# Performance work log

Measured on AMD Instinct MI355X. Metric: run time of the kernel, lower is better.

Reference implementation:

```python
import jax, jax.numpy as jnp
import numpy as np

B, S, H, D, V = 256, 128, 1024, 256, 1858


def setup_inputs() -> dict:
    key = jax.random.key(0)
    ks = jax.random.split(key, 13)
    s = 1.0 / np.sqrt(H)
    return {
        "hidden_states": jax.random.normal(ks[0], (B, S, H), jnp.float32),
        "Wf": jax.random.normal(ks[1], (D, H), jnp.float32) * s,
        "bf": jax.random.normal(ks[2], (D,), jnp.float32) * 0.01,
        "Wt": jax.random.normal(ks[3], (D, H), jnp.float32) * s,
        "bt": jax.random.normal(ks[4], (D,), jnp.float32) * 0.01,
        "Wg": jax.random.normal(ks[5], (D, H), jnp.float32) * s,
        "bg": jax.random.normal(ks[6], (D,), jnp.float32) * 0.01,
        "promo_tab": jax.random.normal(ks[7], (5, D), jnp.float32),
        "Ws": jax.random.normal(ks[8], (1, D), jnp.float32) * (1.0 / np.sqrt(D)),
        "bs": jax.random.normal(ks[9], (1,), jnp.float32) * 0.01,
        "from_sqs": jax.random.randint(ks[10], (V,), 0, 64, jnp.int32),
        "to_sqs": jax.random.randint(ks[11], (V,), 0, 64, jnp.int32),
        "promo_types": jax.random.randint(ks[12], (V,), 0, 5, jnp.int32),
    }


def reference(hidden_states, Wf, bf, Wt, bt, Wg, bg, promo_tab, Ws, bs,
              from_sqs, to_sqs, promo_types):
    # hidden_states: [B, S, H]; squares are tokens 3:67, global token is 0.
    sq_hidden = hidden_states[:, 3:67, :]          # [B, 64, H]
    global_hidden = hidden_states[:, 0, :]         # [B, H]

    # Linear commutes with gather: project the 64 unique squares first,
    # then gather per move (same math as gather-then-project).
    fp = jnp.einsum('bsh,dh->bsd', sq_hidden, Wf) + bf   # [B, 64, D]
    tp = jnp.einsum('bsh,dh->bsd', sq_hidden, Wt) + bt   # [B, 64, D]
    gp = global_hidden @ Wg.T + bg                       # [B, D]

    from_proj = fp[:, from_sqs, :]                       # [B, V, D]
    to_proj = tp[:, to_sqs, :]                           # [B, V, D]
    promo_feats = promo_tab[promo_types]                 # [V, D]

    combined = from_proj * to_proj + gp[:, None, :] + promo_feats[None]
    # score_proj: Linear(D, 1), then squeeze(-1) -> [B, V]
    return jnp.einsum('bvd,d->bv', jax.nn.relu(combined), Ws[0]) + bs[0]
```

## Files before the change

kernel.cpp:

```cpp
#include <hip/hip_runtime.h>

#define NB   256
#define NSQ  64
#define NH   1024
#define ND   256
#define NV   1858
#define M_   (NB * NSQ)
#define N_   512
#define K_   1024
#define NKT  32

typedef __attribute__((ext_vector_type(4))) float f32x4;
typedef __attribute__((ext_vector_type(8))) short bf16x8;
typedef __attribute__((ext_vector_type(8))) unsigned short u16x8;

__device__ __forceinline__ unsigned short bf16_rne(float x) {
    unsigned u = __float_as_uint(x);
    unsigned r = u + 0x7fffu + ((u >> 16) & 1u);
    return (unsigned short)(r >> 16);
}

__device__ __forceinline__ void gload16(const void* g, void* l) {
    __builtin_amdgcn_global_load_lds(
        (const __attribute__((address_space(1))) unsigned int*)g,
        (__attribute__((address_space(3))) unsigned int*)l, 16, 0, 0);
}

__global__ __launch_bounds__(256) void cast_kernel(
    const float* __restrict__ hid,
    const float* __restrict__ Wf, const float* __restrict__ Wt,
    char* __restrict__ Ahi, char* __restrict__ Alo,
    char* __restrict__ Whi, char* __restrict__ Wlo) {
    int bid = blockIdx.x;
    int tid = threadIdx.x;
    int o = tid * 16;
    int g_l = o >> 10;
    int w = o & 1023;
    int s = w >> 8;
    int r = (w >> 4) & 15;
    const float* src;
    char* dh; char* dl;
    if (bid < 8192) {
        int brow = bid >> 5;
        int kt = bid & 31;
        int m = brow * 64 + g_l * 16 + r;
        int b = m >> 6, sr = m & 63;
        int k = kt * 32 + s * 8;
        src = hid + (size_t)(b * 128 + 3 + sr) * NH + k;
        size_t outb = ((size_t)((brow >> 1) * 32 + kt) << 13) + ((brow & 1) << 12) + o;
        dh = Ahi + outb; dl = Alo + outb;
    } else {
        int bid2 = bid - 8192;
        int nrb = bid2 >> 5;
        int kt = bid2 & 31;
        int n = nrb * 64 + g_l * 16 + r;
        int k = kt * 32 + s * 8;
        src = ((n < ND) ? (Wf + (size_t)n * NH) : (Wt + (size_t)(n - ND) * NH)) + k;
        size_t outb = ((size_t)((nrb >> 1) * 32 + kt) << 13) + ((nrb & 1) << 12) + o;
        dh = Whi + outb; dl = Wlo + outb;
    }
    float4 v0 = ((const float4*)src)[0];
    float4 v1 = ((const float4*)src)[1];
    float vv[8] = {v0.x, v0.y, v0.z, v0.w, v1.x, v1.y, v1.z, v1.w};
    u16x8 h, l;
#pragma unroll
    for (int j = 0; j < 8; ++j) {
        unsigned short hb = bf16_rne(vv[j]);
        float hf = __uint_as_float((unsigned)hb << 16);
        h[j] = hb;
        l[j] = bf16_rne(vv[j] - hf);
    }
    *(u16x8*)dh = h;
    *(u16x8*)dl = l;
}

__global__ __launch_bounds__(1024) void gp_kernel(
    const float* __restrict__ hid, const float* __restrict__ Wg,
    const float* __restrict__ bg, float* __restrict__ gp) {
    __shared__ float h[NH];
    int b = blockIdx.x;
    int tid = threadIdx.x;
    if (tid < 256) ((float4*)h)[tid] = ((const float4*)(hid + (size_t)b * 128 * NH))[tid];
    __syncthreads();
    int wave = tid >> 6, lane = tid & 63;
    const float4* hs = (const float4*)h;
    for (int dd = 0; dd < 16; ++dd) {
        int d = wave * 16 + dd;
        const float4* wrow = (const float4*)(Wg + (size_t)d * NH);
        float acc = 0.f;
#pragma unroll
        for (int p = 0; p < 4; ++p) {
            float4 w = wrow[p * 64 + lane];
            float4 x = hs[p * 64 + lane];
            acc += w.x * x.x + w.y * x.y + w.z * x.z + w.w * x.w;
        }
#pragma unroll
        for (int o = 32; o > 0; o >>= 1) acc += __shfl_xor(acc, o, 64);
        if (lane == 0) gp[(size_t)b * ND + d] = acc + bg[d];
    }
}

__global__ __launch_bounds__(256) void gemm3_kernel(
    const char* __restrict__ Ahi, const char* __restrict__ Alo,
    const char* __restrict__ Whi, const char* __restrict__ Wlo,
    const float* __restrict__ bfv, const float* __restrict__ btv,
    float* __restrict__ C) {
    __shared__ unsigned short lAh[128 * 32], lAl[128 * 32];
    __shared__ unsigned short lBh[128 * 32], lBl[128 * 32];
    int tid = threadIdx.x;
    int wgid = (blockIdx.x & 7) * 64 + (blockIdx.x >> 3);
    int nt = wgid & 3;
    int mt = wgid >> 2;
    int lane = tid & 63, wv = tid >> 6;
    int wm = (wv >> 1) * 64, wn = (wv & 1) * 64;
    int fr = lane & 15, kh = lane >> 4;
    f32x4 acc[4][4] = {};

    for (int kt = 0; kt < NKT; ++kt) {
        size_t ta = (size_t)(mt * NKT + kt) << 13;
        size_t tb = (size_t)(nt * NKT + kt) << 13;
#pragma unroll
        for (int is = 0; is < 2; ++is) {
            int o = is * 4096 + tid * 16;
            gload16(Ahi + ta + o, (char*)lAh + o);
            gload16(Alo + ta + o, (char*)lAl + o);
            gload16(Whi + tb + o, (char*)lBh + o);
            gload16(Wlo + tb + o, (char*)lBl + o);
        }
        __syncthreads();
        bf16x8 ah[4], al[4], bh[4], bl[4];
#pragma unroll
        for (int f = 0; f < 4; ++f) {
            int ea = (wm + f * 16) * 32 + kh * 128 + fr * 8;
            int eb = (wn + f * 16) * 32 + kh * 128 + fr * 8;
            ah[f] = *(const bf16x8*)&lAh[ea];
            al[f] = *(const bf16x8*)&lAl[ea];
            bh[f] = *(const bf16x8*)&lBh[eb];
            bl[f] = *(const bf16x8*)&lBl[eb];
        }
#pragma unroll
        for (int i = 0; i < 4; ++i)
#pragma unroll
            for (int j = 0; j < 4; ++j) {
                acc[i][j] = __builtin_amdgcn_mfma_f32_16x16x32_bf16(ah[i], bh[j], acc[i][j], 0, 0, 0);
                acc[i][j] = __builtin_amdgcn_mfma_f32_16x16x32_bf16(ah[i], bl[j], acc[i][j], 0, 0, 0);
                acc[i][j] = __builtin_amdgcn_mfma_f32_16x16x32_bf16(al[i], bh[j], acc[i][j], 0, 0, 0);
            }
        __syncthreads();
    }

    const float* bias = (nt < 2) ? bfv : btv;
    int nb0 = nt * 128 - ((nt < 2) ? 0 : 256);
#pragma unroll
    for (int j = 0; j < 4; ++j) {
        int ncol = nt * 128 + wn + j * 16 + fr;
        float bv = bias[nb0 + wn + j * 16 + fr];
#pragma unroll
        for (int i = 0; i < 4; ++i) {
            int mrow = mt * 128 + wm + i * 16 + kh * 4;
#pragma unroll
            for (int r = 0; r < 4; ++r) {
                C[(size_t)(mrow + r) * N_ + ncol] = acc[i][j][r] + bv;
            }
        }
    }
}

__global__ __launch_bounds__(1024) void out_kernel(
    const float* __restrict__ C, const float* __restrict__ gp,
    const float* __restrict__ promo_tab, const float* __restrict__ Wsv,
    const float* __restrict__ bsv,
    const int* __restrict__ from_sqs, const int* __restrict__ to_sqs,
    const int* __restrict__ ptypes, float* __restrict__ out) {
    __shared__ float cb[NSQ * N_];
    __shared__ float gpl[ND];
    __shared__ float wsl[ND];
    __shared__ float pl[5 * ND];
    __shared__ int fsq[NV], tsq[NV], pty[NV];
    int b = blockIdx.x;
    int tid = threadIdx.x;
    const float4* src = (const float4*)(C + (size_t)b * NSQ * N_);
    float4* dst = (float4*)cb;
#pragma unroll
    for (int i = 0; i < 8; ++i) dst[tid + i * 1024] = src[tid + i * 1024];
    if (tid < 64) ((float4*)gpl)[tid] = ((const float4*)(gp + (size_t)b * ND))[tid];
    else if (tid < 128) ((float4*)wsl)[tid - 64] = ((const float4*)Wsv)[tid - 64];
    else if (tid < 448) ((float4*)pl)[tid - 128] = ((const float4*)promo_tab)[tid - 128];
    for (int v = tid; v < NV; v += 1024) {
        fsq[v] = from_sqs[v];
        tsq[v] = to_sqs[v];
        pty[v] = ptypes[v];
    }
    __syncthreads();

    int wave = tid >> 6, lane = tid & 63;
    float bias0 = bsv[0];
    const float4* cb4 = (const float4*)cb;
    const float4* gp4 = (const float4*)gpl;
    const float4* ws4 = (const float4*)wsl;
    const float4* pl4 = (const float4*)pl;
    for (int v = wave; v < NV; v += 16) {
        int sf = fsq[v];
        int st = tsq[v];
        int p  = pty[v];
        float4 a = cb4[sf * 128 + lane];
        float4 t = cb4[st * 128 + 64 + lane];
        float4 g = gp4[lane];
        float4 pp = pl4[p * 64 + lane];
        float4 w = ws4[lane];
        float c0 = a.x * t.x + g.x + pp.x;
        float c1 = a.y * t.y + g.y + pp.y;
        float c2 = a.z * t.z + g.z + pp.z;
        float c3 = a.w * t.w + g.w + pp.w;
        float s = fmaxf(c0, 0.f) * w.x + fmaxf(c1, 0.f) * w.y +
                  fmaxf(c2, 0.f) * w.z + fmaxf(c3, 0.f) * w.w;
#pragma unroll
        for (int o = 32; o > 0; o >>= 1) s += __shfl_xor(s, o, 64);
        if (lane == 0) out[(size_t)b * NV + v] = s + bias0;
    }
}

extern "C" void kernel_launch(void* const* d_in, const int* in_sizes, int n_in,
                              void* d_out, int out_size, void* d_ws, size_t ws_size,
                              hipStream_t stream) {
    (void)in_sizes; (void)n_in; (void)out_size; (void)ws_size;
    const float* hid   = (const float*)d_in[0];
    const float* Wf    = (const float*)d_in[1];
    const float* bfv   = (const float*)d_in[2];
    const float* Wt    = (const float*)d_in[3];
    const float* btv   = (const float*)d_in[4];
    const float* Wg    = (const float*)d_in[5];
    const float* bgv   = (const float*)d_in[6];
    const float* promo = (const float*)d_in[7];
    const float* Wsv   = (const float*)d_in[8];
    const float* bsv   = (const float*)d_in[9];
    const int* from_sqs = (const int*)d_in[10];
    const int* to_sqs   = (const int*)d_in[11];
    const int* ptypes   = (const int*)d_in[12];
    float* out = (float*)d_out;

    char* ws = (char*)d_ws;
    char* Ahi = ws;
    char* Alo = ws + 33554432;
    char* Whi = ws + 67108864;
    char* Wlo = ws + 68157440;
    float* C  = (float*)(ws + 69206016);
    float* gp = (float*)(ws + 102760448);

    cast_kernel<<<8448, 256, 0, stream>>>(hid, Wf, Wt, Ahi, Alo, Whi, Wlo);
    gp_kernel<<<256, 1024, 0, stream>>>(hid, Wg, bgv, gp);
    gemm3_kernel<<<512, 256, 0, stream>>>(Ahi, Alo, Whi, Wlo, bfv, btv, C);
    out_kernel<<<256, 1024, 0, stream>>>(C, gp, promo, Wsv, bsv,
                                         from_sqs, to_sqs, ptypes, out);
}
```

Baseline: 336.0 us.

## Pipeline bf16x3 GEMM with triple-buffered LDS and 256x128 tiles

Restructures the split-bf16 GEMM so each 512-thread block computes a 256x128 tile, with 8 waves sharing one B tile. Global-to-LDS loads run through a three-stage ring buffer that prefetches two K-steps ahead. Those loads are interleaved between MFMA groups using barriers, setprio and sched_barrier. The aim is to hide global load latency and cut B-tile traffic, at the cost of 144KB of LDS (one block per CU) and half as many blocks.

```diff
diff --git a/kernel.cpp b/kernel.cpp
--- a/kernel.cpp
+++ b/kernel.cpp
@@ -9,6 +9,7 @@
 #define N_   512
 #define K_   1024
 #define NKT  32
+#define BUFB 49152
 
 typedef __attribute__((ext_vector_type(4))) float f32x4;
 typedef __attribute__((ext_vector_type(8))) short bf16x8;
@@ -100,70 +101,146 @@
     }
 }
 
-__global__ __launch_bounds__(256) void gemm3_kernel(
+__global__ __launch_bounds__(512) void gemm3_kernel(
     const char* __restrict__ Ahi, const char* __restrict__ Alo,
     const char* __restrict__ Whi, const char* __restrict__ Wlo,
     const float* __restrict__ bfv, const float* __restrict__ btv,
     float* __restrict__ C) {
-    __shared__ unsigned short lAh[128 * 32], lAl[128 * 32];
-    __shared__ unsigned short lBh[128 * 32], lBl[128 * 32];
+    __shared__ char lds[3 * BUFB];
     int tid = threadIdx.x;
-    int wgid = (blockIdx.x & 7) * 64 + (blockIdx.x >> 3);
+    int lane = tid & 63, wv = tid >> 6;
+    int wgid = (blockIdx.x & 7) * 32 + (blockIdx.x >> 3);
     int nt = wgid & 3;
     int mt = wgid >> 2;
-    int lane = tid & 63, wv = tid >> 6;
-    int wm = (wv >> 1) * 64, wn = (wv & 1) * 64;
+    int wm = wv >> 1;
+    int wnw = wv & 1;
     int fr = lane & 15, kh = lane >> 4;
+
+    const char* gsrc[6];
+    int loff[6];
+#pragma unroll
+    for (int l = 0; l < 6; ++l) {
+        int seg = wv * 6 + l;
+        const char* base; int lo;
+        if (seg < 8)       { base = Ahi + ((size_t)((2*mt)*NKT) << 13)   + seg*1024;      lo = seg*1024; }
+        else if (seg < 16) { base = Ahi + ((size_t)((2*mt+1)*NKT) << 13) + (seg-8)*1024;  lo = 8192  + (seg-8)*1024; }
+        else if (seg < 24) { base = Alo + ((size_t)((2*mt)*NKT) << 13)   + (seg-16)*1024; lo = 16384 + (seg-16)*1024; }
+        else if (seg < 32) { base = Alo + ((size_t)((2*mt+1)*NKT) << 13) + (seg-24)*1024; lo = 24576 + (seg-24)*1024; }
+        else if (seg < 40) { base = Whi + ((size_t)(nt*NKT) << 13)       + (seg-32)*1024; lo = 32768 + (seg-32)*1024; }
+        else               { base = Wlo + ((size_t)(nt*NKT) << 13)       + (seg-40)*1024; lo = 40960 + (seg-40)*1024; }
+        gsrc[l] = base + lane * 16;
+        loff[l] = lo + lane * 16;
+    }
+
+#define STG(l, ktn, sb) gload16(gsrc[l] + ((size_t)(ktn) << 13), lds + (sb) * BUFB + loff[l])
+
     f32x4 acc[4][4] = {};
 
-    for (int kt = 0; kt < NKT; ++kt) {
-        size_t ta = (size_t)(mt * NKT + kt) << 13;
-        size_t tb = (size_t)(nt * NKT + kt) << 13;
-#pragma unroll
-        for (int is = 0; is < 2; ++is) {
-            int o = is * 4096 + tid * 16;
-            gload16(Ahi + ta + o, (char*)lAh + o);
-            gload16(Alo + ta + o, (char*)lAl + o);
-            gload16(Whi + tb + o, (char*)lBh + o);
-            gload16(Wlo + tb + o, (char*)lBl + o);
-        }
-        __syncthreads();
-        bf16x8 ah[4], al[4], bh[4], bl[4];
-#pragma unroll
-        for (int f = 0; f < 4; ++f) {
-            int ea = (wm + f * 16) * 32 + kh * 128 + fr * 8;
-            int eb = (wn + f * 16) * 32 + kh * 128 + fr * 8;
-            ah[f] = *(const bf16x8*)&lAh[ea];
-            al[f] = *(const bf16x8*)&lAl[ea];
-            bh[f] = *(const bf16x8*)&lBh[eb];
-            bl[f] = *(const bf16x8*)&lBl[eb];
-        }
-#pragma unroll
-        for (int i = 0; i < 4; ++i)
-#pragma unroll
-            for (int j = 0; j < 4; ++j) {
-                acc[i][j] = __builtin_amdgcn_mfma_f32_16x16x32_bf16(ah[i], bh[j], acc[i][j], 0, 0, 0);
-                acc[i][j] = __builtin_amdgcn_mfma_f32_16x16x32_bf16(ah[i], bl[j], acc[i][j], 0, 0, 0);
-                acc[i][j] = __builtin_amdgcn_mfma_f32_16x16x32_bf16(al[i], bh[j], acc[i][j], 0, 0, 0);
-            }
-        __syncthreads();
+#pragma unroll
+    for (int l = 0; l < 6; ++l) STG(l, 0, 0);
+#pragma unroll
+    for (int l = 0; l < 6; ++l) STG(l, 1, 1);
+    asm volatile("s_waitcnt vmcnt(6)" ::: "memory");
+    __builtin_amdgcn_s_barrier();
+    __builtin_amdgcn_sched_barrier(0);
+
+    int rcur = 0, snext = 2;
+    int aoff0 = (wm >> 1) * 8192 + (wm & 1) * 4096 + kh * 256 + fr * 16;
+    int boff0 = 32768 + wnw * 4096 + kh * 256 + fr * 16;
+
+#pragma unroll 1
+    for (int t = 0; t < NKT; ++t) {
+        const char* cb = lds + rcur * BUFB;
+        int ktn = (t + 2) & (NKT - 1);
+        bf16x8 bh[4], bl[4];
+
+#pragma unroll
+        for (int j = 0; j < 4; ++j) {
+            bh[j] = *(const bf16x8*)(cb + boff0 + j * 1024);
+            bl[j] = *(const bf16x8*)(cb + boff0 + 8192 + j * 1024);
+        }
+        bf16x8 ah0 = *(const bf16x8*)(cb + aoff0);
+        bf16x8 al0 = *(const bf16x8*)(cb + 16384 + aoff0);
+        STG(0, ktn, snext); STG(1, ktn, snext);
+        __builtin_amdgcn_s_barrier();
+        __builtin_amdgcn_s_setprio(1);
+#pragma unroll
+        for (int j = 0; j < 4; ++j) {
+            acc[0][j] = __builtin_amdgcn_mfma_f32_16x16x32_bf16(ah0, bh[j], acc[0][j], 0, 0, 0);
+            acc[0][j] = __builtin_amdgcn_mfma_f32_16x16x32_bf16(ah0, bl[j], acc[0][j], 0, 0, 0);
+            acc[0][j] = __builtin_amdgcn_mfma_f32_16x16x32_bf16(al0, bh[j], acc[0][j], 0, 0, 0);
+        }
+        __builtin_amdgcn_s_setprio(0);
+        __builtin_amdgcn_s_barrier();
+        __builtin_amdgcn_sched_barrier(0);
+
+        bf16x8 ah1 = *(const bf16x8*)(cb + aoff0 + 1024);
+        bf16x8 al1 = *(const bf16x8*)(cb + 16384 + aoff0 + 1024);
+        STG(2, ktn, snext); STG(3, ktn, snext);
+        __builtin_amdgcn_s_barrier();
+        __builtin_amdgcn_s_setprio(1);
+#pragma unroll
+        for (int j = 0; j < 4; ++j) {
+            acc[1][j] = __builtin_amdgcn_mfma_f32_16x16x32_bf16(ah1, bh[j], acc[1][j], 0, 0, 0);
+            acc[1][j] = __builtin_amdgcn_mfma_f32_16x16x32_bf16(ah1, bl[j], acc[1][j], 0, 0, 0);
+            acc[1][j] = __builtin_amdgcn_mfma_f32_16x16x32_bf16(al1, bh[j], acc[1][j], 0, 0, 0);
+        }
+        __builtin_amdgcn_s_setprio(0);
+        __builtin_amdgcn_s_barrier();
+        __builtin_amdgcn_sched_barrier(0);
+
+        bf16x8 ah2 = *(const bf16x8*)(cb + aoff0 + 2048);
+        bf16x8 al2 = *(const bf16x8*)(cb + 16384 + aoff0 + 2048);
+        STG(4, ktn, snext);
+        __builtin_amdgcn_s_barrier();
+        __builtin_amdgcn_s_setprio(1);
+#pragma unroll
+        for (int j = 0; j < 4; ++j) {
+            acc[2][j] = __builtin_amdgcn_mfma_f32_16x16x32_bf16(ah2, bh[j], acc[2][j], 0, 0, 0);
+            acc[2][j] = __builtin_amdgcn_mfma_f32_16x16x32_bf16(ah2, bl[j], acc[2][j], 0, 0, 0);
+            acc[2][j] = __builtin_amdgcn_mfma_f32_16x16x32_bf16(al2, bh[j], acc[2][j], 0, 0, 0);
+        }
+        __builtin_amdgcn_s_setprio(0);
+        __builtin_amdgcn_s_barrier();
+        __builtin_amdgcn_sched_barrier(0);
+
+        bf16x8 ah3 = *(const bf16x8*)(cb + aoff0 + 3072);
+        bf16x8 al3 = *(const bf16x8*)(cb + 16384 + aoff0 + 3072);
+        STG(5, ktn, snext);
+        __builtin_amdgcn_s_barrier();
+        __builtin_amdgcn_s_setprio(1);
+#pragma unroll
+        for (int j = 0; j < 4; ++j) {
+            acc[3][j] = __builtin_amdgcn_mfma_f32_16x16x32_bf16(ah3, bh[j], acc[3][j], 0, 0, 0);
+            acc[3][j] = __builtin_amdgcn_mfma_f32_16x16x32_bf16(ah3, bl[j], acc[3][j], 0, 0, 0);
+            acc[3][j] = __builtin_amdgcn_mfma_f32_16x16x32_bf16(al3, bh[j], acc[3][j], 0, 0, 0);
+        }
+        __builtin_amdgcn_s_setprio(0);
+        asm volatile("s_waitcnt vmcnt(6)" ::: "memory");
+        __builtin_amdgcn_s_barrier();
+        __builtin_amdgcn_sched_barrier(0);
+
+        rcur = (rcur == 2) ? 0 : rcur + 1;
+        snext = (snext == 2) ? 0 : snext + 1;
     }
 
     const float* bias = (nt < 2) ? bfv : btv;
     int nb0 = nt * 128 - ((nt < 2) ? 0 : 256);
 #pragma unroll
     for (int j = 0; j < 4; ++j) {
-        int ncol = nt * 128 + wn + j * 16 + fr;
-        float bv = bias[nb0 + wn + j * 16 + fr];
+        int nc = wnw * 64 + j * 16 + fr;
+        int ncol = nt * 128 + nc;
+        float bv = bias[nb0 + nc];
 #pragma unroll
         for (int i = 0; i < 4; ++i) {
-            int mrow = mt * 128 + wm + i * 16 + kh * 4;
+            int mrow = mt * 256 + wm * 64 + i * 16 + kh * 4;
 #pragma unroll
             for (int r = 0; r < 4; ++r) {
                 C[(size_t)(mrow + r) * N_ + ncol] = acc[i][j][r] + bv;
             }
         }
     }
+#undef STG
 }
 
 __global__ __launch_bounds__(1024) void out_kernel(
@@ -249,7 +326,7 @@
 
     cast_kernel<<<8448, 256, 0, stream>>>(hid, Wf, Wt, Ahi, Alo, Whi, Wlo);
     gp_kernel<<<256, 1024, 0, stream>>>(hid, Wg, bgv, gp);
-    gemm3_kernel<<<512, 256, 0, stream>>>(Ahi, Alo, Whi, Wlo, bfv, btv, C);
+    gemm3_kernel<<<256, 512, 0, stream>>>(Ahi, Alo, Whi, Wlo, bfv, btv, C);
     out_kernel<<<256, 1024, 0, stream>>>(C, gp, promo, Wsv, bsv,
                                          from_sqs, to_sqs, ptypes, out);
 }
```

Measured after the change: 334.4 us. No clear change (-0.5%).

## Fuse activation cast, GEMM and scoring into one per-batch kernel

Applied to the files above, without the earlier changes.

Removes the separate activation cast pass and the C intermediate buffer. One block per batch now converts hidden rows to bf16 hi/lo pairs in registers, writes them to LDS, and runs a double-buffered split-bf16 MFMA GEMM for all 512 output columns. It then keeps the projections in LDS for the gather/ReLU/dot scoring stage. This cuts global traffic heavily, but only 256 blocks of 512 threads with about 144KB of LDS each can run, so occupancy drops and each block does much more serial work.

```diff
diff --git a/kernel.cpp b/kernel.cpp
--- a/kernel.cpp
+++ b/kernel.cpp
@@ -5,9 +5,7 @@
 #define NH   1024
 #define ND   256
 #define NV   1858
-#define M_   (NB * NSQ)
 #define N_   512
-#define K_   1024
 #define NKT  32
 
 typedef __attribute__((ext_vector_type(4))) float f32x4;
@@ -26,10 +24,8 @@
         (__attribute__((address_space(3))) unsigned int*)l, 16, 0, 0);
 }
 
-__global__ __launch_bounds__(256) void cast_kernel(
-    const float* __restrict__ hid,
+__global__ __launch_bounds__(256) void cast_W_kernel(
     const float* __restrict__ Wf, const float* __restrict__ Wt,
-    char* __restrict__ Ahi, char* __restrict__ Alo,
     char* __restrict__ Whi, char* __restrict__ Wlo) {
     int bid = blockIdx.x;
     int tid = threadIdx.x;
@@ -38,27 +34,11 @@
     int w = o & 1023;
     int s = w >> 8;
     int r = (w >> 4) & 15;
-    const float* src;
-    char* dh; char* dl;
-    if (bid < 8192) {
-        int brow = bid >> 5;
-        int kt = bid & 31;
-        int m = brow * 64 + g_l * 16 + r;
-        int b = m >> 6, sr = m & 63;
-        int k = kt * 32 + s * 8;
-        src = hid + (size_t)(b * 128 + 3 + sr) * NH + k;
-        size_t outb = ((size_t)((brow >> 1) * 32 + kt) << 13) + ((brow & 1) << 12) + o;
-        dh = Ahi + outb; dl = Alo + outb;
-    } else {
-        int bid2 = bid - 8192;
-        int nrb = bid2 >> 5;
-        int kt = bid2 & 31;
-        int n = nrb * 64 + g_l * 16 + r;
-        int k = kt * 32 + s * 8;
-        src = ((n < ND) ? (Wf + (size_t)n * NH) : (Wt + (size_t)(n - ND) * NH)) + k;
-        size_t outb = ((size_t)((nrb >> 1) * 32 + kt) << 13) + ((nrb & 1) << 12) + o;
-        dh = Whi + outb; dl = Wlo + outb;
-    }
+    int nrb = bid >> 5, kt = bid & 31;
+    int n = nrb * 64 + g_l * 16 + r;
+    int k = kt * 32 + s * 8;
+    const float* src = ((n < ND) ? (Wf + (size_t)n * NH) : (Wt + (size_t)(n - ND) * NH)) + k;
+    size_t outb = ((size_t)((nrb >> 1) * 32 + kt) << 13) + ((nrb & 1) << 12) + o;
     float4 v0 = ((const float4*)src)[0];
     float4 v1 = ((const float4*)src)[1];
     float vv[8] = {v0.x, v0.y, v0.z, v0.w, v1.x, v1.y, v1.z, v1.w};
@@ -70,8 +50,8 @@
         h[j] = hb;
         l[j] = bf16_rne(vv[j] - hf);
     }
-    *(u16x8*)dh = h;
-    *(u16x8*)dl = l;
+    *(u16x8*)(Whi + outb) = h;
+    *(u16x8*)(Wlo + outb) = l;
 }
 
 __global__ __launch_bounds__(1024) void gp_kernel(
@@ -100,124 +80,147 @@
     }
 }
 
-__global__ __launch_bounds__(256) void gemm3_kernel(
-    const char* __restrict__ Ahi, const char* __restrict__ Alo,
+__global__ __launch_bounds__(512) void fused_kernel(
+    const float* __restrict__ hid,
     const char* __restrict__ Whi, const char* __restrict__ Wlo,
     const float* __restrict__ bfv, const float* __restrict__ btv,
-    float* __restrict__ C) {
-    __shared__ unsigned short lAh[128 * 32], lAl[128 * 32];
-    __shared__ unsigned short lBh[128 * 32], lBl[128 * 32];
-    int tid = threadIdx.x;
-    int wgid = (blockIdx.x & 7) * 64 + (blockIdx.x >> 3);
-    int nt = wgid & 3;
-    int mt = wgid >> 2;
-    int lane = tid & 63, wv = tid >> 6;
-    int wm = (wv >> 1) * 64, wn = (wv & 1) * 64;
-    int fr = lane & 15, kh = lane >> 4;
-    f32x4 acc[4][4] = {};
-
-    for (int kt = 0; kt < NKT; ++kt) {
-        size_t ta = (size_t)(mt * NKT + kt) << 13;
-        size_t tb = (size_t)(nt * NKT + kt) << 13;
-#pragma unroll
-        for (int is = 0; is < 2; ++is) {
-            int o = is * 4096 + tid * 16;
-            gload16(Ahi + ta + o, (char*)lAh + o);
-            gload16(Alo + ta + o, (char*)lAl + o);
-            gload16(Whi + tb + o, (char*)lBh + o);
-            gload16(Wlo + tb + o, (char*)lBl + o);
-        }
-        __syncthreads();
-        bf16x8 ah[4], al[4], bh[4], bl[4];
-#pragma unroll
-        for (int f = 0; f < 4; ++f) {
-            int ea = (wm + f * 16) * 32 + kh * 128 + fr * 8;
-            int eb = (wn + f * 16) * 32 + kh * 128 + fr * 8;
-            ah[f] = *(const bf16x8*)&lAh[ea];
-            al[f] = *(const bf16x8*)&lAl[ea];
-            bh[f] = *(const bf16x8*)&lBh[eb];
-            bl[f] = *(const bf16x8*)&lBl[eb];
-        }
-#pragma unroll
-        for (int i = 0; i < 4; ++i)
-#pragma unroll
-            for (int j = 0; j < 4; ++j) {
-                acc[i][j] = __builtin_amdgcn_mfma_f32_16x16x32_bf16(ah[i], bh[j], acc[i][j], 0, 0, 0);
-                acc[i][j] = __builtin_amdgcn_mfma_f32_16x16x32_bf16(ah[i], bl[j], acc[i][j], 0, 0, 0);
-                acc[i][j] = __builtin_amdgcn_mfma_f32_16x16x32_bf16(al[i], bh[j], acc[i][j], 0, 0, 0);
-            }
-        __syncthreads();
-    }
-
-    const float* bias = (nt < 2) ? bfv : btv;
-    int nb0 = nt * 128 - ((nt < 2) ? 0 : 256);
-#pragma unroll
-    for (int j = 0; j < 4; ++j) {
-        int ncol = nt * 128 + wn + j * 16 + fr;
-        float bv = bias[nb0 + wn + j * 16 + fr];
-#pragma unroll
-        for (int i = 0; i < 4; ++i) {
-            int mrow = mt * 128 + wm + i * 16 + kh * 4;
-#pragma unroll
-            for (int r = 0; r < 4; ++r) {
-                C[(size_t)(mrow + r) * N_ + ncol] = acc[i][j][r] + bv;
-            }
-        }
-    }
-}
-
-__global__ __launch_bounds__(1024) void out_kernel(
-    const float* __restrict__ C, const float* __restrict__ gp,
-    const float* __restrict__ promo_tab, const float* __restrict__ Wsv,
-    const float* __restrict__ bsv,
+    const float* __restrict__ gp, const float* __restrict__ promo,
+    const float* __restrict__ Wsv, const float* __restrict__ bsv,
     const int* __restrict__ from_sqs, const int* __restrict__ to_sqs,
     const int* __restrict__ ptypes, float* __restrict__ out) {
-    __shared__ float cb[NSQ * N_];
-    __shared__ float gpl[ND];
-    __shared__ float wsl[ND];
-    __shared__ float pl[5 * ND];
-    __shared__ int fsq[NV], tsq[NV], pty[NV];
-    int b = blockIdx.x;
-    int tid = threadIdx.x;
-    const float4* src = (const float4*)(C + (size_t)b * NSQ * N_);
-    float4* dst = (float4*)cb;
-#pragma unroll
-    for (int i = 0; i < 8; ++i) dst[tid + i * 1024] = src[tid + i * 1024];
+    __shared__ __align__(16) char lds[147456];
+    const int tid = threadIdx.x;
+    const int lane = tid & 63, wv = tid >> 6;
+    const int fr = lane & 15, kh = lane >> 4;
+    const int b = blockIdx.x;
+
+    const int arow = tid >> 3, ak4 = tid & 7;
+    const float* asrc = hid + (size_t)(b * 128 + 3 + arow) * NH + ak4 * 4;
+    const int awoff = 131072 + (arow >> 4) * 1024 + (ak4 >> 1) * 256 +
+                      (arow & 15) * 16 + (ak4 & 1) * 8;
+
+    const int bbase = (wv >> 1) * 8192 + (wv & 1) * 4096 + kh * 256 + fr * 16;
+    const int abase = 131072 + kh * 256 + fr * 16;
+
+#define BSTG(kt, p)                                                              \
+    do {                                                                         \
+        _Pragma("unroll") for (int l = 0; l < 4; ++l) {                          \
+            gload16(Whi + (((size_t)(l * NKT + (kt))) << 13) + tid * 16,         \
+                    lds + (p) * 65536 + l * 8192 + tid * 16);                    \
+            gload16(Wlo + (((size_t)(l * NKT + (kt))) << 13) + tid * 16,         \
+                    lds + (p) * 65536 + 32768 + l * 8192 + tid * 16);            \
+        }                                                                        \
+    } while (0)
+
+    f32x4 acc[4][4] = {};
+
+    BSTG(0, 0);
+    __builtin_amdgcn_sched_barrier(0);
+    float4 a_cur = *(const float4*)(asrc);
+    __builtin_amdgcn_sched_barrier(0);
+    BSTG(1, 1);
+    __builtin_amdgcn_sched_barrier(0);
+    float4 a_nxt = *(const float4*)(asrc + 32);
+    __builtin_amdgcn_sched_barrier(0);
+
+#pragma unroll 1
+    for (int t = 0; t < NKT; ++t) {
+        const int p = t & 1;
+        ushort4 h4, l4;
+        {
+            h4.x = bf16_rne(a_cur.x);
+            l4.x = bf16_rne(a_cur.x - __uint_as_float((unsigned)h4.x << 16));
+            h4.y = bf16_rne(a_cur.y);
+            l4.y = bf16_rne(a_cur.y - __uint_as_float((unsigned)h4.y << 16));
+            h4.z = bf16_rne(a_cur.z);
+            l4.z = bf16_rne(a_cur.z - __uint_as_float((unsigned)h4.z << 16));
+            h4.w = bf16_rne(a_cur.w);
+            l4.w = bf16_rne(a_cur.w - __uint_as_float((unsigned)h4.w << 16));
+        }
+        *(ushort4*)(lds + awoff + p * 8192) = h4;
+        *(ushort4*)(lds + awoff + p * 8192 + 4096) = l4;
+        asm volatile("s_waitcnt vmcnt(9)" ::: "memory");
+        asm volatile("s_waitcnt lgkmcnt(0)" ::: "memory");
+        asm volatile("s_barrier" ::: "memory");
+
+        const char* bb = lds + p * 65536;
+        bf16x8 bh[4], bl[4];
+#pragma unroll
+        for (int j = 0; j < 4; ++j) {
+            bh[j] = *(const bf16x8*)(bb + bbase + j * 1024);
+            bl[j] = *(const bf16x8*)(bb + bbase + 32768 + j * 1024);
+        }
+        __builtin_amdgcn_s_setprio(1);
+#pragma unroll
+        for (int i = 0; i < 4; ++i) {
+            bf16x8 ah = *(const bf16x8*)(lds + abase + p * 8192 + i * 1024);
+            bf16x8 al = *(const bf16x8*)(lds + abase + p * 8192 + 4096 + i * 1024);
+#pragma unroll
+            for (int j = 0; j < 4; ++j) {
+                acc[i][j] = __builtin_amdgcn_mfma_f32_16x16x32_bf16(ah, bh[j], acc[i][j], 0, 0, 0);
+                acc[i][j] = __builtin_amdgcn_mfma_f32_16x16x32_bf16(ah, bl[j], acc[i][j], 0, 0, 0);
+                acc[i][j] = __builtin_amdgcn_mfma_f32_16x16x32_bf16(al, bh[j], acc[i][j], 0, 0, 0);
+            }
+        }
+        __builtin_amdgcn_s_setprio(0);
+        asm volatile("s_barrier" ::: "memory");
+
+        const int ktn = (t + 2) & (NKT - 1);
+        BSTG(ktn, p);
+        __builtin_amdgcn_sched_barrier(0);
+        a_cur = a_nxt;
+        a_nxt = *(const float4*)(asrc + ktn * 32);
+        __builtin_amdgcn_sched_barrier(0);
+    }
+
+    asm volatile("s_waitcnt vmcnt(0) lgkmcnt(0)" ::: "memory");
+    asm volatile("s_barrier" ::: "memory");
+
+    float* cb = (float*)lds;
+#pragma unroll
+    for (int j = 0; j < 4; ++j) {
+        int col = wv * 64 + j * 16 + fr;
+        float bv = (col < ND) ? bfv[col] : btv[col - ND];
+#pragma unroll
+        for (int i = 0; i < 4; ++i) {
+            int row = i * 16 + kh * 4;
+#pragma unroll
+            for (int r = 0; r < 4; ++r)
+                cb[(row + r) * N_ + col] = acc[i][j][r] + bv;
+        }
+    }
+    float* gpl = (float*)(lds + 131072);
+    float* wsl = (float*)(lds + 132096);
+    float* pl  = (float*)(lds + 133120);
     if (tid < 64) ((float4*)gpl)[tid] = ((const float4*)(gp + (size_t)b * ND))[tid];
     else if (tid < 128) ((float4*)wsl)[tid - 64] = ((const float4*)Wsv)[tid - 64];
-    else if (tid < 448) ((float4*)pl)[tid - 128] = ((const float4*)promo_tab)[tid - 128];
-    for (int v = tid; v < NV; v += 1024) {
-        fsq[v] = from_sqs[v];
-        tsq[v] = to_sqs[v];
-        pty[v] = ptypes[v];
-    }
-    __syncthreads();
-
-    int wave = tid >> 6, lane = tid & 63;
+    else if (tid < 448) ((float4*)pl)[tid - 128] = ((const float4*)promo)[tid - 128];
+    asm volatile("s_waitcnt lgkmcnt(0)" ::: "memory");
+    asm volatile("s_barrier" ::: "memory");
+
+    const float4* cb4 = (const float4*)lds;
+    const float4* pl4 = (const float4*)pl;
+    float4 g4 = ((const float4*)gpl)[lane];
+    float4 w4 = ((const float4*)wsl)[lane];
     float bias0 = bsv[0];
-    const float4* cb4 = (const float4*)cb;
-    const float4* gp4 = (const float4*)gpl;
-    const float4* ws4 = (const float4*)wsl;
-    const float4* pl4 = (const float4*)pl;
-    for (int v = wave; v < NV; v += 16) {
-        int sf = fsq[v];
-        int st = tsq[v];
-        int p  = pty[v];
-        float4 a = cb4[sf * 128 + lane];
-        float4 t = cb4[st * 128 + 64 + lane];
-        float4 g = gp4[lane];
-        float4 pp = pl4[p * 64 + lane];
-        float4 w = ws4[lane];
-        float c0 = a.x * t.x + g.x + pp.x;
-        float c1 = a.y * t.y + g.y + pp.y;
-        float c2 = a.z * t.z + g.z + pp.z;
-        float c3 = a.w * t.w + g.w + pp.w;
-        float s = fmaxf(c0, 0.f) * w.x + fmaxf(c1, 0.f) * w.y +
-                  fmaxf(c2, 0.f) * w.z + fmaxf(c3, 0.f) * w.w;
+    for (int v = wv; v < NV; v += 8) {
+        int sf = from_sqs[v];
+        int st = to_sqs[v];
+        int pt = ptypes[v];
+        float4 a  = cb4[sf * 128 + lane];
+        float4 t4 = cb4[st * 128 + 64 + lane];
+        float4 pp = pl4[pt * 64 + lane];
+        float c0 = a.x * t4.x + g4.x + pp.x;
+        float c1 = a.y * t4.y + g4.y + pp.y;
+        float c2 = a.z * t4.z + g4.z + pp.z;
+        float c3 = a.w * t4.w + g4.w + pp.w;
+        float s = fmaxf(c0, 0.f) * w4.x + fmaxf(c1, 0.f) * w4.y +
+                  fmaxf(c2, 0.f) * w4.z + fmaxf(c3, 0.f) * w4.w;
 #pragma unroll
         for (int o = 32; o > 0; o >>= 1) s += __shfl_xor(s, o, 64);
         if (lane == 0) out[(size_t)b * NV + v] = s + bias0;
     }
+#undef BSTG
 }
 
 extern "C" void kernel_launch(void* const* d_in, const int* in_sizes, int n_in,
@@ -240,16 +243,13 @@
     float* out = (float*)d_out;
 
     char* ws = (char*)d_ws;
-    char* Ahi = ws;
-    char* Alo = ws + 33554432;
-    char* Whi = ws + 67108864;
-    char* Wlo = ws + 68157440;
-    float* C  = (float*)(ws + 69206016);
-    float* gp = (float*)(ws + 102760448);
-
-    cast_kernel<<<8448, 256, 0, stream>>>(hid, Wf, Wt, Ahi, Alo, Whi, Wlo);
+    char* Whi = ws;
+    char* Wlo = ws + 1048576;
+    float* gp = (float*)(ws + 2097152);
+
+    cast_W_kernel<<<256, 256, 0, stream>>>(Wf, Wt, Whi, Wlo);
     gp_kernel<<<256, 1024, 0, stream>>>(hid, Wg, bgv, gp);
-    gemm3_kernel<<<512, 256, 0, stream>>>(Ahi, Alo, Whi, Wlo, bfv, btv, C);
-    out_kernel<<<256, 1024, 0, stream>>>(C, gp, promo, Wsv, bsv,
-                                         from_sqs, to_sqs, ptypes, out);
-}
+    fused_kernel<<<256, 512, 0, stream>>>(hid, Whi, Wlo, bfv, btv, gp,
+                                          promo, Wsv, bsv,
+                                          from_sqs, to_sqs, ptypes, out);
+}
```

Measured after the change: 381.6 us. 13.6% more time.

## Fuse activation bf16 hi/lo split into GEMM and drop A staging buffers

Applied to the files above, without the earlier changes.

The separate cast pass that split hidden states into bf16 hi/lo tiles in workspace is removed. The GEMM now reads fp32 hidden rows directly, splits them in registers and writes both halves to LDS, with the next k-tile's fp32 loads issued during the MFMA phase as a register prefetch. This removes a 64 MB write plus read-back of the A operand. In exchange it adds VALU conversion work and register pressure inside the GEMM main loop, and the weight cast now runs as its own small kernel.

```diff
diff --git a/kernel.cpp b/kernel.cpp
--- a/kernel.cpp
+++ b/kernel.cpp
@@ -7,7 +7,6 @@
 #define NV   1858
 #define M_   (NB * NSQ)
 #define N_   512
-#define K_   1024
 #define NKT  32
 
 typedef __attribute__((ext_vector_type(4))) float f32x4;
@@ -26,10 +25,19 @@
         (__attribute__((address_space(3))) unsigned int*)l, 16, 0, 0);
 }
 
-__global__ __launch_bounds__(256) void cast_kernel(
-    const float* __restrict__ hid,
+__device__ __forceinline__ void split8(const float4 a, const float4 b,
+                                       u16x8& hi, u16x8& lo) {
+    float vv[8] = {a.x, a.y, a.z, a.w, b.x, b.y, b.z, b.w};
+#pragma unroll
+    for (int j = 0; j < 8; ++j) {
+        unsigned short hb = bf16_rne(vv[j]);
+        hi[j] = hb;
+        lo[j] = bf16_rne(vv[j] - __uint_as_float((unsigned)hb << 16));
+    }
+}
+
+__global__ __launch_bounds__(256) void cast_W_kernel(
     const float* __restrict__ Wf, const float* __restrict__ Wt,
-    char* __restrict__ Ahi, char* __restrict__ Alo,
     char* __restrict__ Whi, char* __restrict__ Wlo) {
     int bid = blockIdx.x;
     int tid = threadIdx.x;
@@ -38,40 +46,17 @@
     int w = o & 1023;
     int s = w >> 8;
     int r = (w >> 4) & 15;
-    const float* src;
-    char* dh; char* dl;
-    if (bid < 8192) {
-        int brow = bid >> 5;
-        int kt = bid & 31;
-        int m = brow * 64 + g_l * 16 + r;
-        int b = m >> 6, sr = m & 63;
-        int k = kt * 32 + s * 8;
-        src = hid + (size_t)(b * 128 + 3 + sr) * NH + k;
-        size_t outb = ((size_t)((brow >> 1) * 32 + kt) << 13) + ((brow & 1) << 12) + o;
-        dh = Ahi + outb; dl = Alo + outb;
-    } else {
-        int bid2 = bid - 8192;
-        int nrb = bid2 >> 5;
-        int kt = bid2 & 31;
-        int n = nrb * 64 + g_l * 16 + r;
-        int k = kt * 32 + s * 8;
-        src = ((n < ND) ? (Wf + (size_t)n * NH) : (Wt + (size_t)(n - ND) * NH)) + k;
-        size_t outb = ((size_t)((nrb >> 1) * 32 + kt) << 13) + ((nrb & 1) << 12) + o;
-        dh = Whi + outb; dl = Wlo + outb;
-    }
+    int nrb = bid >> 5, kt = bid & 31;
+    int n = nrb * 64 + g_l * 16 + r;
+    int k = kt * 32 + s * 8;
+    const float* src = ((n < ND) ? (Wf + (size_t)n * NH) : (Wt + (size_t)(n - ND) * NH)) + k;
+    size_t outb = ((size_t)((nrb >> 1) * 32 + kt) << 13) + ((nrb & 1) << 12) + o;
     float4 v0 = ((const float4*)src)[0];
     float4 v1 = ((const float4*)src)[1];
-    float vv[8] = {v0.x, v0.y, v0.z, v0.w, v1.x, v1.y, v1.z, v1.w};
     u16x8 h, l;
-#pragma unroll
-    for (int j = 0; j < 8; ++j) {
-        unsigned short hb = bf16_rne(vv[j]);
-        float hf = __uint_as_float((unsigned)hb << 16);
-        h[j] = hb;
-        l[j] = bf16_rne(vv[j] - hf);
-    }
-    *(u16x8*)dh = h;
-    *(u16x8*)dl = l;
+    split8(v0, v1, h, l);
+    *(u16x8*)(Whi + outb) = h;
+    *(u16x8*)(Wlo + outb) = l;
 }
 
 __global__ __launch_bounds__(1024) void gp_kernel(
@@ -100,43 +85,68 @@
     }
 }
 
-__global__ __launch_bounds__(256) void gemm3_kernel(
-    const char* __restrict__ Ahi, const char* __restrict__ Alo,
+__global__ __launch_bounds__(256) void gemm3f_kernel(
+    const float* __restrict__ hid,
     const char* __restrict__ Whi, const char* __restrict__ Wlo,
     const float* __restrict__ bfv, const float* __restrict__ btv,
     float* __restrict__ C) {
-    __shared__ unsigned short lAh[128 * 32], lAl[128 * 32];
-    __shared__ unsigned short lBh[128 * 32], lBl[128 * 32];
-    int tid = threadIdx.x;
+    __shared__ __align__(16) char lA[16384];
+    __shared__ __align__(16) char lB[16384];
+    int tid = threadIdx.x;
+    int lane = tid & 63, wv = tid >> 6;
     int wgid = (blockIdx.x & 7) * 64 + (blockIdx.x >> 3);
     int nt = wgid & 3;
     int mt = wgid >> 2;
-    int lane = tid & 63, wv = tid >> 6;
     int wm = (wv >> 1) * 64, wn = (wv & 1) * 64;
     int fr = lane & 15, kh = lane >> 4;
+
+    int r = tid >> 1, h = tid & 1;
+    const float* asrc = hid +
+        (size_t)((2 * mt + (r >> 6)) * 128 + 3 + (r & 63)) * NH + h * 16;
+    int awb = (r >> 4) * 1024 + h * 512 + (r & 15) * 16;
+
+    const char* bsrch = Whi + ((size_t)(nt * NKT) << 13) + tid * 16;
+    const char* bsrcl = Wlo + ((size_t)(nt * NKT) << 13) + tid * 16;
+
     f32x4 acc[4][4] = {};
+    float4 va0, va1, va2, va3, vn0, vn1, vn2, vn3;
+    va0 = ((const float4*)asrc)[0];
+    va1 = ((const float4*)asrc)[1];
+    va2 = ((const float4*)asrc)[2];
+    va3 = ((const float4*)asrc)[3];
 
     for (int kt = 0; kt < NKT; ++kt) {
-        size_t ta = (size_t)(mt * NKT + kt) << 13;
-        size_t tb = (size_t)(nt * NKT + kt) << 13;
-#pragma unroll
-        for (int is = 0; is < 2; ++is) {
-            int o = is * 4096 + tid * 16;
-            gload16(Ahi + ta + o, (char*)lAh + o);
-            gload16(Alo + ta + o, (char*)lAl + o);
-            gload16(Whi + tb + o, (char*)lBh + o);
-            gload16(Wlo + tb + o, (char*)lBl + o);
-        }
+        size_t tb = (size_t)kt << 13;
+        gload16(bsrch + tb, lB + tid * 16);
+        gload16(bsrch + tb + 4096, lB + 4096 + tid * 16);
+        gload16(bsrcl + tb, lB + 8192 + tid * 16);
+        gload16(bsrcl + tb + 4096, lB + 12288 + tid * 16);
+
+        u16x8 h0, h1, l0, l1;
+        split8(va0, va1, h0, l0);
+        split8(va2, va3, h1, l1);
+        *(u16x8*)(lA + awb) = h0;
+        *(u16x8*)(lA + awb + 256) = h1;
+        *(u16x8*)(lA + 8192 + awb) = l0;
+        *(u16x8*)(lA + 8192 + awb + 256) = l1;
         __syncthreads();
+
+        int ktn = (kt + 1) & (NKT - 1);
+        const float* an = asrc + ktn * 32;
+        vn0 = ((const float4*)an)[0];
+        vn1 = ((const float4*)an)[1];
+        vn2 = ((const float4*)an)[2];
+        vn3 = ((const float4*)an)[3];
+
         bf16x8 ah[4], al[4], bh[4], bl[4];
 #pragma unroll
         for (int f = 0; f < 4; ++f) {
-            int ea = (wm + f * 16) * 32 + kh * 128 + fr * 8;
-            int eb = (wn + f * 16) * 32 + kh * 128 + fr * 8;
-            ah[f] = *(const bf16x8*)&lAh[ea];
-            al[f] = *(const bf16x8*)&lAl[ea];
-            bh[f] = *(const bf16x8*)&lBh[eb];
-            bl[f] = *(const bf16x8*)&lBl[eb];
+            int ea = (wm + f * 16) * 64 + kh * 256 + fr * 16;
+            int eb = (wn + f * 16) * 64 + kh * 256 + fr * 16;
+            ah[f] = *(const bf16x8*)(lA + ea);
+            al[f] = *(const bf16x8*)(lA + 8192 + ea);
+            bh[f] = *(const bf16x8*)(lB + eb);
+            bl[f] = *(const bf16x8*)(lB + 8192 + eb);
         }
 #pragma unroll
         for (int i = 0; i < 4; ++i)
@@ -147,6 +157,7 @@
                 acc[i][j] = __builtin_amdgcn_mfma_f32_16x16x32_bf16(al[i], bh[j], acc[i][j], 0, 0, 0);
             }
         __syncthreads();
+        va0 = vn0; va1 = vn1; va2 = vn2; va3 = vn3;
     }
 
     const float* bias = (nt < 2) ? bfv : btv;
@@ -159,8 +170,8 @@
         for (int i = 0; i < 4; ++i) {
             int mrow = mt * 128 + wm + i * 16 + kh * 4;
 #pragma unroll
-            for (int r = 0; r < 4; ++r) {
-                C[(size_t)(mrow + r) * N_ + ncol] = acc[i][j][r] + bv;
+            for (int rr = 0; rr < 4; ++rr) {
+                C[(size_t)(mrow + rr) * N_ + ncol] = acc[i][j][rr] + bv;
             }
         }
     }
@@ -240,16 +251,14 @@
     float* out = (float*)d_out;
 
     char* ws = (char*)d_ws;
-    char* Ahi = ws;
-    char* Alo = ws + 33554432;
-    char* Whi = ws + 67108864;
-    char* Wlo = ws + 68157440;
-    float* C  = (float*)(ws + 69206016);
-    float* gp = (float*)(ws + 102760448);
-
-    cast_kernel<<<8448, 256, 0, stream>>>(hid, Wf, Wt, Ahi, Alo, Whi, Wlo);
+    char* Whi = ws;
+    char* Wlo = ws + 1048576;
+    float* C  = (float*)(ws + 2097152);
+    float* gp = (float*)(ws + 35651584);
+
+    cast_W_kernel<<<256, 256, 0, stream>>>(Wf, Wt, Whi, Wlo);
     gp_kernel<<<256, 1024, 0, stream>>>(hid, Wg, bgv, gp);
-    gemm3_kernel<<<512, 256, 0, stream>>>(Ahi, Alo, Whi, Wlo, bfv, btv, C);
+    gemm3f_kernel<<<512, 256, 0, stream>>>(hid, Whi, Wlo, bfv, btv, C);
     out_kernel<<<256, 1024, 0, stream>>>(C, gp, promo, Wsv, bsv,
                                          from_sqs, to_sqs, ptypes, out);
 }
```

Result: faster. 328.7 us (-2.2%).
